# Performance work log

Hardware: AMD Instinct MI355X
Metric: run time of the kernel (lower is better)

Reference implementation:

```python
import jax, jax.numpy as jnp
import numpy as np

B = 32768


def _mk(key, shape, scale=0.05):
    return (jax.random.normal(key, shape, dtype=jnp.float32) * scale)


def setup_inputs() -> dict:
    key = jax.random.key(0)
    ks = jax.random.split(key, 24)
    inp = {
        "p_i": jax.random.normal(ks[0], (B, 512), dtype=jnp.float32),
        "speed": jax.random.normal(ks[1], (B,), dtype=jnp.float32),
        "command": jax.random.randint(ks[2], (B,), 0, 4),
        "sp_W1": _mk(ks[3], (1, 128)), "sp_b1": jnp.zeros((128,), jnp.float32),
        "sp_W2": _mk(ks[4], (128, 128)), "sp_b2": jnp.zeros((128,), jnp.float32),
        "sp_W3": _mk(ks[5], (128, 128)), "sp_b3": jnp.zeros((128,), jnp.float32),
        # speed_pred_module: 512 -> 128 -> 128 -> 1
        "vp_W1": _mk(ks[6], (512, 128)), "vp_b1": jnp.zeros((128,), jnp.float32),
        "vp_W2": _mk(ks[7], (128, 128)), "vp_b2": jnp.zeros((128,), jnp.float32),
        "vp_W3": _mk(ks[8], (128, 1)), "vp_b3": jnp.zeros((1,), jnp.float32),
        # join_module: Linear(640, 512)
        "join_W": _mk(ks[9], (640, 512)), "join_b": jnp.zeros((512,), jnp.float32),
        # 4 control heads: 512 -> 256 -> 256 -> 3 (stacked over expert axis e)
        "ctrl_W1": _mk(ks[10], (4, 512, 256)), "ctrl_b1": jnp.zeros((4, 256), jnp.float32),
        "ctrl_W2": _mk(ks[11], (4, 256, 256)), "ctrl_b2": jnp.zeros((4, 256), jnp.float32),
        "ctrl_W3": _mk(ks[12], (4, 256, 3)), "ctrl_b3": jnp.zeros((4, 3), jnp.float32),
    }
    return inp


def _mlp3(x, W1, b1, W2, b2, W3, b3):
    h = jax.nn.relu(x @ W1 + b1)
    h = jax.nn.relu(h @ W2 + b2)
    return h @ W3 + b3


def reference(p_i, speed, command,
              sp_W1, sp_b1, sp_W2, sp_b2, sp_W3, sp_b3,
              vp_W1, vp_b1, vp_W2, vp_b2, vp_W3, vp_b3,
              join_W, join_b,
              ctrl_W1, ctrl_b1, ctrl_W2, ctrl_b2, ctrl_W3, ctrl_b3):
    v = _mlp3(speed[:, None], sp_W1, sp_b1, sp_W2, sp_b2, sp_W3, sp_b3)
    # join: [B, 640] -> [B, 512]
    joined = jnp.concatenate([p_i, v], axis=1) @ join_W + join_b
    # speed prediction [B,1]
    v_p = _mlp3(p_i, vp_W1, vp_b1, vp_W2, vp_b2, vp_W3, vp_b3)
    # command-indexed routing: compute all 4 tiny heads batched, then select.
    h = jax.nn.relu(jnp.einsum('bd,edh->beh', joined, ctrl_W1) + ctrl_b1)  # [B,4,256]
    h = jax.nn.relu(jnp.einsum('beh,ehk->bek', h, ctrl_W2) + ctrl_b2)      # [B,4,256]
    a = jnp.einsum('beh,ehk->bek', h, ctrl_W3) + ctrl_b3                    # [B,4,3]
    action = jnp.take_along_axis(a, command[:, None, None], axis=1)[:, 0, :]  # [B,3]
    return (v_p, action)
```

## Files before the change

kernel.cpp:

```cpp
#include <hip/hip_runtime.h>
#include <stdint.h>

#define NROWS 32768

typedef float f32x4 __attribute__((ext_vector_type(4)));
typedef __bf16 bfx8 __attribute__((ext_vector_type(8)));
typedef unsigned uint4v __attribute__((ext_vector_type(4)));

static __device__ __forceinline__ unsigned short f2bf(float f) {
    unsigned u = __builtin_bit_cast(unsigned, f);
    u += 0x7fffu + ((u >> 16) & 1u);
    return (unsigned short)(u >> 16);
}

static __device__ __forceinline__ f32x4 mfma16(bfx8 a, bfx8 b, f32x4 c) {
    return __builtin_amdgcn_mfma_f32_16x16x32_bf16(a, b, c, 0, 0, 0);
}

static __device__ __forceinline__ int swz(int row, int col) {
    return col ^ ((row & 7) << 3);
}

static constexpr size_t A_AUG_B  = 0;
static constexpr size_t JOINED_B = 41943040;
static constexpr size_t G1_B     = 75497472;
static constexpr size_t WCT_B    = 83886080;
static constexpr size_t SPW2T_B  = 84705280;
static constexpr size_t SPW3T_B  = 84738048;
static constexpr size_t VPW2T_B  = 84770816;
static constexpr size_t VPW3T_B  = 84803584;
static constexpr size_t C1T_B    = 84807680;
static constexpr size_t C2T_B    = 85856256;
static constexpr size_t C3T_B    = 86380544;
static constexpr size_t CNT_B    = 86413312;
static constexpr size_t SORTED_B = 86413376;
static constexpr size_t WS_NEED  = 86937664;

__global__ __launch_bounds__(256) void k_prep(
    const float* joinW, const float* vpW1, const float* spW2, const float* spW3,
    const float* vpW2, const float* vpW3, const float* c1, const float* c2, const float* c3,
    unsigned short* wct, unsigned short* spw2t, unsigned short* spw3t,
    unsigned short* vpw2t, unsigned short* vpw3t,
    unsigned short* c1t, unsigned short* c2t, unsigned short* c3t, int* cnt)
{
    int bid = blockIdx.x, tid = threadIdx.x;
    if (bid == 0 && tid < 16) cnt[tid] = 0;
    int region, idx0;
    if      (bid < 400)  { region = 0; idx0 = bid * 1024; }
    else if (bid < 416)  { region = 1; idx0 = (bid - 400) * 1024; }
    else if (bid < 432)  { region = 2; idx0 = (bid - 416) * 1024; }
    else if (bid < 448)  { region = 3; idx0 = (bid - 432) * 1024; }
    else if (bid < 450)  { region = 4; idx0 = (bid - 448) * 1024; }
    else if (bid < 962)  { region = 5; idx0 = (bid - 450) * 1024; }
    else if (bid < 1218) { region = 6; idx0 = (bid - 962) * 1024; }
    else                 { region = 7; idx0 = (bid - 1218) * 1024; }
    for (int j = 0; j < 4; ++j) {
        int idx = idx0 + tid + j * 256;
        switch (region) {
        case 0: {
            int n = idx / 640, k = idx % 640;
            float v = (n < 512) ? joinW[(size_t)k * 512 + n]
                                : (k < 512 ? vpW1[(size_t)k * 128 + (n - 512)] : 0.f);
            wct[idx] = f2bf(v);
        } break;
        case 1: { int n = idx >> 7, k = idx & 127; spw2t[idx] = f2bf(spW2[k * 128 + n]); } break;
        case 2: { int n = idx >> 7, k = idx & 127; spw3t[idx] = f2bf(spW3[k * 128 + n]); } break;
        case 3: { int n = idx >> 7, k = idx & 127; vpw2t[idx] = f2bf(vpW2[k * 128 + n]); } break;
        case 4: { int n = idx >> 7, k = idx & 127; vpw3t[idx] = f2bf(n == 0 ? vpW3[k] : 0.f); } break;
        case 5: { int e = idx >> 17, rem = idx & 131071, n = rem >> 9, k = rem & 511;
                  c1t[idx] = f2bf(c1[(size_t)e * 131072 + k * 256 + n]); } break;
        case 6: { int e = idx >> 16, rem = idx & 65535, n = rem >> 8, k = rem & 255;
                  c2t[idx] = f2bf(c2[(size_t)e * 65536 + k * 256 + n]); } break;
        case 7: { int e = idx >> 12, rem = idx & 4095, n = rem >> 8, k = rem & 255;
                  c3t[idx] = f2bf(n < 3 ? c3[(size_t)e * 768 + k * 3 + n] : 0.f); } break;
        }
    }
}

__global__ __launch_bounds__(256) void k_sp_convert(
    const float* p_i, const float* speed, const float* spW1, const float* spb1,
    const float* spb2, const float* spb3,
    const unsigned short* spw2t, const unsigned short* spw3t, unsigned short* Aaug)
{
    __shared__ alignas(16) unsigned short h1[128 * 128];
    __shared__ alignas(16) unsigned short h2[128 * 128];
    int bid = blockIdx.x, tid = threadIdx.x;
    int r0 = bid * 128;
#pragma unroll 4
    for (int j = 0; j < 64; ++j) {
        int c = tid + j * 256;
        int row = c >> 7, col4 = (c & 127) * 4;
        f32x4 v = *(const f32x4*)(p_i + (size_t)(r0 + row) * 512 + col4);
        ushort4 o;
        o.x = f2bf(v.x); o.y = f2bf(v.y); o.z = f2bf(v.z); o.w = f2bf(v.w);
        *(ushort4*)(Aaug + (size_t)(r0 + row) * 640 + col4) = o;
    }
    for (int j = 0; j < 64; ++j) {
        int idx = tid + j * 256;
        int row = idx >> 7, col = idx & 127;
        float h = speed[r0 + row] * spW1[col] + spb1[col];
        h = h > 0.f ? h : 0.f;
        h1[row * 128 + swz(row, col)] = f2bf(h);
    }
    __syncthreads();

    int wave = tid >> 6, lane = tid & 63, lq = lane >> 4, lr = lane & 15;
    int wr = wave >> 1, wc = wave & 1;
    f32x4 acc[4][4] = {};
#pragma unroll
    for (int ks = 0; ks < 4; ++ks) {
        bfx8 a[4], b[4];
#pragma unroll
        for (int mt = 0; mt < 4; ++mt) {
            int row = wr * 64 + mt * 16 + lr;
            a[mt] = *(const bfx8*)&h1[row * 128 + swz(row, ks * 32 + lq * 8)];
        }
#pragma unroll
        for (int nt = 0; nt < 4; ++nt) {
            int n = wc * 64 + nt * 16 + lr;
            b[nt] = *(const bfx8*)(spw2t + n * 128 + ks * 32 + lq * 8);
        }
#pragma unroll
        for (int mt = 0; mt < 4; ++mt)
#pragma unroll
            for (int nt = 0; nt < 4; ++nt)
                acc[mt][nt] = mfma16(a[mt], b[nt], acc[mt][nt]);
    }
#pragma unroll
    for (int mt = 0; mt < 4; ++mt)
#pragma unroll
        for (int nt = 0; nt < 4; ++nt)
#pragma unroll
            for (int j = 0; j < 4; ++j) {
                int row = wr * 64 + mt * 16 + lq * 4 + j;
                int col = wc * 64 + nt * 16 + lr;
                float v = acc[mt][nt][j] + spb2[col];
                v = v > 0.f ? v : 0.f;
                h2[row * 128 + swz(row, col)] = f2bf(v);
            }
    __syncthreads();
    f32x4 acc2[4][4] = {};
#pragma unroll
    for (int ks = 0; ks < 4; ++ks) {
        bfx8 a[4], b[4];
#pragma unroll
        for (int mt = 0; mt < 4; ++mt) {
            int row = wr * 64 + mt * 16 + lr;
            a[mt] = *(const bfx8*)&h2[row * 128 + swz(row, ks * 32 + lq * 8)];
        }
#pragma unroll
        for (int nt = 0; nt < 4; ++nt) {
            int n = wc * 64 + nt * 16 + lr;
            b[nt] = *(const bfx8*)(spw3t + n * 128 + ks * 32 + lq * 8);
        }
#pragma unroll
        for (int mt = 0; mt < 4; ++mt)
#pragma unroll
            for (int nt = 0; nt < 4; ++nt)
                acc2[mt][nt] = mfma16(a[mt], b[nt], acc2[mt][nt]);
    }
#pragma unroll
    for (int mt = 0; mt < 4; ++mt)
#pragma unroll
        for (int nt = 0; nt < 4; ++nt)
#pragma unroll
            for (int j = 0; j < 4; ++j) {
                int row = wr * 64 + mt * 16 + lq * 4 + j;
                int col = wc * 64 + nt * 16 + lr;
                Aaug[(size_t)(r0 + row) * 640 + 512 + col] = f2bf(acc2[mt][nt][j] + spb3[col]);
            }
}

__global__ __launch_bounds__(256) void k_scatter(const int* command, int* cnt, int* sorted)
{
    __shared__ int lcnt[4], lbase[4];
    int tid = threadIdx.x;
    int r = blockIdx.x * 256 + tid;
    if (tid < 4) lcnt[tid] = 0;
    __syncthreads();
    int c = command[r] & 3;
    int lpos = atomicAdd(&lcnt[c], 1);
    __syncthreads();
    if (tid < 4) lbase[tid] = atomicAdd(&cnt[tid], lcnt[tid]);
    __syncthreads();
    sorted[c * NROWS + lbase[c] + lpos] = r;
}

__global__ __launch_bounds__(256) void k_join(
    const unsigned short* Aaug, const unsigned short* wct,
    const float* joinb, const float* vpb1, unsigned short* joined, unsigned short* g1)
{
    __shared__ alignas(16) unsigned short At[128 * 64];
    __shared__ alignas(16) unsigned short Bt[128 * 64];
    int d = blockIdx.x;
    int L = (d & 7) * 160 + (d >> 3);
    int m0 = (L / 5) * 128, n0 = (L % 5) * 128;
    int tid = threadIdx.x, wave = tid >> 6, lane = tid & 63, lq = lane >> 4, lr = lane & 15;
    int wr = wave >> 1, wc = wave & 1;
    f32x4 acc[4][4] = {};
#pragma unroll 1
    for (int kt = 0; kt < 10; ++kt) {
#pragma unroll
        for (int c2 = 0; c2 < 4; ++c2) {
            int chunk = c2 * 256 + tid;
            int row = chunk >> 3, slot = chunk & 7;
            uint4v va = *(const uint4v*)(Aaug + (size_t)(m0 + row) * 640 + kt * 64 + slot * 8);
            uint4v vb = *(const uint4v*)(wct + (size_t)(n0 + row) * 640 + kt * 64 + slot * 8);
            *(uint4v*)&At[chunk * 8] = va;
            *(uint4v*)&Bt[chunk * 8] = vb;
        }
        __syncthreads();
#pragma unroll
        for (int ks = 0; ks < 2; ++ks) {
            bfx8 a[4], b[4];
#pragma unroll
            for (int mt = 0; mt < 4; ++mt)
                a[mt] = *(const bfx8*)&At[(wr * 64 + mt * 16 + lr) * 64 + ks * 32 + lq * 8];
#pragma unroll
            for (int nt = 0; nt < 4; ++nt)
                b[nt] = *(const bfx8*)&Bt[(wc * 64 + nt * 16 + lr) * 64 + ks * 32 + lq * 8];
#pragma unroll
            for (int mt = 0; mt < 4; ++mt)
#pragma unroll
                for (int nt = 0; nt < 4; ++nt)
                    acc[mt][nt] = mfma16(a[mt], b[nt], acc[mt][nt]);
        }
        __syncthreads();
    }
#pragma unroll
    for (int mt = 0; mt < 4; ++mt)
#pragma unroll
        for (int nt = 0; nt < 4; ++nt)
#pragma unroll
            for (int j = 0; j < 4; ++j) {
                int row = m0 + wr * 64 + mt * 16 + lq * 4 + j;
                int col = n0 + wc * 64 + nt * 16 + lr;
                float v = acc[mt][nt][j];
                if (col < 512) {
                    joined[(size_t)row * 512 + col] = f2bf(v + joinb[col]);
                } else {
                    v += vpb1[col - 512];
                    v = v > 0.f ? v : 0.f;
                    g1[(size_t)row * 128 + (col - 512)] = f2bf(v);
                }
            }
}

__global__ __launch_bounds__(256) void k_vp(
    const unsigned short* g1, const unsigned short* vpw2t, const unsigned short* vpw3t,
    const float* vpb2, const float* vpb3, float* out_vp)
{
    __shared__ alignas(16) unsigned short gt[128 * 128];
    __shared__ alignas(16) unsigned short h2[128 * 128];
    int bid = blockIdx.x, tid = threadIdx.x;
    int r0 = bid * 128;
#pragma unroll
    for (int c2 = 0; c2 < 8; ++c2) {
        int chunk = c2 * 256 + tid;
        int row = chunk >> 4, slot = chunk & 15;
        int sslot = slot ^ (row & 7);
        uint4v v = *(const uint4v*)(g1 + (size_t)(r0 + row) * 128 + slot * 8);
        *(uint4v*)&gt[row * 128 + sslot * 8] = v;
    }
    __syncthreads();
    int wave = tid >> 6, lane = tid & 63, lq = lane >> 4, lr = lane & 15;
    int wr = wave >> 1, wc = wave & 1;
    f32x4 acc[4][4] = {};
#pragma unroll
    for (int ks = 0; ks < 4; ++ks) {
        bfx8 a[4], b[4];
#pragma unroll
        for (int mt = 0; mt < 4; ++mt) {
            int row = wr * 64 + mt * 16 + lr;
            a[mt] = *(const bfx8*)&gt[row * 128 + swz(row, ks * 32 + lq * 8)];
        }
#pragma unroll
        for (int nt = 0; nt < 4; ++nt) {
            int n = wc * 64 + nt * 16 + lr;
            b[nt] = *(const bfx8*)(vpw2t + n * 128 + ks * 32 + lq * 8);
        }
#pragma unroll
        for (int mt = 0; mt < 4; ++mt)
#pragma unroll
            for (int nt = 0; nt < 4; ++nt)
                acc[mt][nt] = mfma16(a[mt], b[nt], acc[mt][nt]);
    }
#pragma unroll
    for (int mt = 0; mt < 4; ++mt)
#pragma unroll
        for (int nt = 0; nt < 4; ++nt)
#pragma unroll
            for (int j = 0; j < 4; ++j) {
                int row = wr * 64 + mt * 16 + lq * 4 + j;
                int col = wc * 64 + nt * 16 + lr;
                float v = acc[mt][nt][j] + vpb2[col];
                v = v > 0.f ? v : 0.f;
                h2[row * 128 + swz(row, col)] = f2bf(v);
            }
    __syncthreads();
    f32x4 acc2[2] = {};
#pragma unroll
    for (int ks = 0; ks < 4; ++ks) {
        bfx8 b = *(const bfx8*)(vpw3t + lr * 128 + ks * 32 + lq * 8);
#pragma unroll
        for (int mt = 0; mt < 2; ++mt) {
            int row = wave * 32 + mt * 16 + lr;
            bfx8 a = *(const bfx8*)&h2[row * 128 + swz(row, ks * 32 + lq * 8)];
            acc2[mt] = mfma16(a, b, acc2[mt]);
        }
    }
    if (lr == 0) {
#pragma unroll
        for (int mt = 0; mt < 2; ++mt)
#pragma unroll
            for (int j = 0; j < 4; ++j) {
                int row = wave * 32 + mt * 16 + lq * 4 + j;
                out_vp[r0 + row] = acc2[mt][j] + vpb3[0];
            }
    }
}

__global__ __launch_bounds__(512) void k_ctrl(
    const unsigned short* joined, const unsigned short* c1t, const unsigned short* c2t,
    const unsigned short* c3t, const float* b1, const float* b2, const float* b3,
    const int* cnt, const int* sorted, float* out_act)
{
    __shared__ alignas(16) unsigned short hls[128 * 256];
    __shared__ alignas(16) unsigned short Ast[128 * 64];
    __shared__ alignas(16) unsigned short Bst[256 * 64];
    __shared__ int ridx[128];
    int bid = blockIdx.x;
    int e = bid >> 8, i = bid & 255;
    int n_e = cnt[e];
    if (i * 128 >= n_e) return;
    int tid = threadIdx.x;
    if (tid < 128) {
        int g = i * 128 + tid;
        ridx[tid] = sorted[e * NROWS + (g < n_e ? g : n_e - 1)];
    }
    __syncthreads();
    int wave = tid >> 6, lane = tid & 63, lq = lane >> 4, lr = lane & 15;
    int wm = wave & 1, wn = wave >> 1;
    const unsigned short* W1 = c1t + e * (256 * 512);
    const unsigned short* W2 = c2t + e * (256 * 256);
    const unsigned short* W3 = c3t + e * (16 * 256);

    f32x4 acc[4][4] = {};
#pragma unroll 1
    for (int kt = 0; kt < 8; ++kt) {
#pragma unroll
        for (int it = 0; it < 2; ++it) {
            int idx = it * 512 + tid;
            int row = idx >> 3, slot = idx & 7;
            uint4v v = *(const uint4v*)(joined + (size_t)ridx[row] * 512 + kt * 64 + slot * 8);
            *(uint4v*)&Ast[row * 64 + (slot ^ (row & 7)) * 8] = v;
        }
#pragma unroll
        for (int it = 0; it < 4; ++it) {
            int idx = it * 512 + tid;
            int n = idx >> 3, slot = idx & 7;
            uint4v v = *(const uint4v*)(W1 + (size_t)n * 512 + kt * 64 + slot * 8);
            *(uint4v*)&Bst[n * 64 + (slot ^ (n & 7)) * 8] = v;
        }
        __syncthreads();
#pragma unroll
        for (int ks = 0; ks < 2; ++ks) {
            bfx8 a[4], b[4];
#pragma unroll
            for (int mt = 0; mt < 4; ++mt) {
                int row = wm * 64 + mt * 16 + lr;
                a[mt] = *(const bfx8*)&Ast[row * 64 + ((ks * 32 + lq * 8) ^ ((row & 7) << 3))];
            }
#pragma unroll
            for (int nt = 0; nt < 4; ++nt) {
                int n = wn * 64 + nt * 16 + lr;
                b[nt] = *(const bfx8*)&Bst[n * 64 + ((ks * 32 + lq * 8) ^ ((n & 7) << 3))];
            }
#pragma unroll
            for (int mt = 0; mt < 4; ++mt)
#pragma unroll
                for (int nt = 0; nt < 4; ++nt)
                    acc[mt][nt] = mfma16(a[mt], b[nt], acc[mt][nt]);
        }
        __syncthreads();
    }
#pragma unroll
    for (int mt = 0; mt < 4; ++mt)
#pragma unroll
        for (int nt = 0; nt < 4; ++nt)
#pragma unroll
            for (int j = 0; j < 4; ++j) {
                int row = wm * 64 + mt * 16 + lq * 4 + j;
                int col = wn * 64 + nt * 16 + lr;
                float v = acc[mt][nt][j] + b1[e * 256 + col];
                v = v > 0.f ? v : 0.f;
                hls[row * 256 + swz(row, col)] = f2bf(v);
            }
    __syncthreads();

    f32x4 acc2[4][4] = {};
#pragma unroll 1
    for (int kt = 0; kt < 4; ++kt) {
#pragma unroll
        for (int it = 0; it < 4; ++it) {
            int idx = it * 512 + tid;
            int n = idx >> 3, slot = idx & 7;
            uint4v v = *(const uint4v*)(W2 + (size_t)n * 256 + kt * 64 + slot * 8);
            *(uint4v*)&Bst[n * 64 + (slot ^ (n & 7)) * 8] = v;
        }
        __syncthreads();
#pragma unroll
        for (int ks = 0; ks < 2; ++ks) {
            bfx8 a[4], b[4];
#pragma unroll
            for (int mt = 0; mt < 4; ++mt) {
                int row = wm * 64 + mt * 16 + lr;
                a[mt] = *(const bfx8*)&hls[row * 256 + swz(row, kt * 64 + ks * 32 + lq * 8)];
            }
#pragma unroll
            for (int nt = 0; nt < 4; ++nt) {
                int n = wn * 64 + nt * 16 + lr;
                b[nt] = *(const bfx8*)&Bst[n * 64 + ((ks * 32 + lq * 8) ^ ((n & 7) << 3))];
            }
#pragma unroll
            for (int mt = 0; mt < 4; ++mt)
#pragma unroll
                for (int nt = 0; nt < 4; ++nt)
                    acc2[mt][nt] = mfma16(a[mt], b[nt], acc2[mt][nt]);
        }
        __syncthreads();
    }
#pragma unroll
    for (int mt = 0; mt < 4; ++mt)
#pragma unroll
        for (int nt = 0; nt < 4; ++nt)
#pragma unroll
            for (int j = 0; j < 4; ++j) {
                int row = wm * 64 + mt * 16 + lq * 4 + j;
                int col = wn * 64 + nt * 16 + lr;
                float v = acc2[mt][nt][j] + b2[e * 256 + col];
                v = v > 0.f ? v : 0.f;
                hls[row * 256 + swz(row, col)] = f2bf(v);
            }
    __syncthreads();

    {
        f32x4 acc3 = {};
#pragma unroll
        for (int ks = 0; ks < 8; ++ks) {
            int row = wave * 16 + lr;
            bfx8 a = *(const bfx8*)&hls[row * 256 + swz(row, ks * 32 + lq * 8)];
            bfx8 b = *(const bfx8*)(W3 + lr * 256 + ks * 32 + lq * 8);
            acc3 = mfma16(a, b, acc3);
        }
#pragma unroll
        for (int j = 0; j < 4; ++j) {
            int row = wave * 16 + lq * 4 + j;
            int g = i * 128 + row;
            if (lr < 3 && g < n_e)
                out_act[(size_t)ridx[row] * 3 + lr] = acc3[j] + b3[e * 3 + lr];
        }
    }
}

extern "C" void kernel_launch(void* const* d_in, const int* in_sizes, int n_in,
                              void* d_out, int out_size, void* d_ws, size_t ws_size,
                              hipStream_t stream) {
    (void)in_sizes; (void)n_in; (void)out_size;
    if (ws_size < WS_NEED) return;

    const float* p_i    = (const float*)d_in[0];
    const float* speed  = (const float*)d_in[1];
    const int*   command= (const int*)d_in[2];
    const float* sp_W1  = (const float*)d_in[3];
    const float* sp_b1  = (const float*)d_in[4];
    const float* sp_W2  = (const float*)d_in[5];
    const float* sp_b2  = (const float*)d_in[6];
    const float* sp_W3  = (const float*)d_in[7];
    const float* sp_b3  = (const float*)d_in[8];
    const float* vp_W1  = (const float*)d_in[9];
    const float* vp_b1  = (const float*)d_in[10];
    const float* vp_W2  = (const float*)d_in[11];
    const float* vp_b2  = (const float*)d_in[12];
    const float* vp_W3  = (const float*)d_in[13];
    const float* vp_b3  = (const float*)d_in[14];
    const float* join_W = (const float*)d_in[15];
    const float* join_b = (const float*)d_in[16];
    const float* ctrl_W1= (const float*)d_in[17];
    const float* ctrl_b1= (const float*)d_in[18];
    const float* ctrl_W2= (const float*)d_in[19];
    const float* ctrl_b2= (const float*)d_in[20];
    const float* ctrl_W3= (const float*)d_in[21];
    const float* ctrl_b3= (const float*)d_in[22];

    char* ws = (char*)d_ws;
    unsigned short* Aaug   = (unsigned short*)(ws + A_AUG_B);
    unsigned short* joined = (unsigned short*)(ws + JOINED_B);
    unsigned short* g1     = (unsigned short*)(ws + G1_B);
    unsigned short* wct    = (unsigned short*)(ws + WCT_B);
    unsigned short* spw2t  = (unsigned short*)(ws + SPW2T_B);
    unsigned short* spw3t  = (unsigned short*)(ws + SPW3T_B);
    unsigned short* vpw2t  = (unsigned short*)(ws + VPW2T_B);
    unsigned short* vpw3t  = (unsigned short*)(ws + VPW3T_B);
    unsigned short* c1t    = (unsigned short*)(ws + C1T_B);
    unsigned short* c2t    = (unsigned short*)(ws + C2T_B);
    unsigned short* c3t    = (unsigned short*)(ws + C3T_B);
    int* cnt    = (int*)(ws + CNT_B);
    int* sorted = (int*)(ws + SORTED_B);

    float* out_vp  = (float*)d_out;
    float* out_act = out_vp + NROWS;

    k_prep<<<1234, 256, 0, stream>>>(join_W, vp_W1, sp_W2, sp_W3, vp_W2, vp_W3,
                                     ctrl_W1, ctrl_W2, ctrl_W3,
                                     wct, spw2t, spw3t, vpw2t, vpw3t, c1t, c2t, c3t, cnt);
    k_sp_convert<<<256, 256, 0, stream>>>(p_i, speed, sp_W1, sp_b1, sp_b2, sp_b3,
                                          spw2t, spw3t, Aaug);
    k_scatter<<<128, 256, 0, stream>>>(command, cnt, sorted);
    k_join<<<1280, 256, 0, stream>>>(Aaug, wct, join_b, vp_b1, joined, g1);
    k_vp<<<256, 256, 0, stream>>>(g1, vpw2t, vpw3t, vp_b2, vp_b3, out_vp);
    k_ctrl<<<1024, 512, 0, stream>>>(joined, c1t, c2t, c3t, ctrl_b1, ctrl_b2, ctrl_b3,
                                     cnt, sorted, out_act);
}
```

Before: 317.8 us.

## Prefetch next K-tile into registers and XOR-swizzle LDS tiles in join GEMM

The join GEMM kernel now loads the next K-tile from global memory into registers while the current tile is being consumed by MFMAs, so global-load latency overlaps compute instead of sitting before each barrier. LDS stores and fragment reads use an XOR swizzle on the 16-byte slot index, keyed by row, to avoid bank conflicts on the strided bfx8 reads. This raises register pressure with eight extra uint4 prefetch registers per thread, which could reduce occupancy.

```diff
diff --git a/kernel.cpp b/kernel.cpp
--- a/kernel.cpp
+++ b/kernel.cpp
@@ -197,28 +197,49 @@
     int m0 = (L / 5) * 128, n0 = (L % 5) * 128;
     int tid = threadIdx.x, wave = tid >> 6, lane = tid & 63, lq = lane >> 4, lr = lane & 15;
     int wr = wave >> 1, wc = wave & 1;
+
+    int r0t = tid >> 3, s0t = tid & 7;
+    int ss = s0t ^ (r0t & 7);
+    const unsigned short* aब = Aaug + (size_t)(m0 + r0t) * 640 + s0t * 8;
+    const unsigned short* bब = wct + (size_t)(n0 + r0t) * 640 + s0t * 8;
+    unsigned short* lA = &At[r0t * 64 + ss * 8];
+    unsigned short* lB = &Bt[r0t * 64 + ss * 8];
+
+    uint4v ra[4], rb[4];
+#pragma unroll
+    for (int c2 = 0; c2 < 4; ++c2) {
+        ra[c2] = *(const uint4v*)(aब + c2 * (32 * 640));
+        rb[c2] = *(const uint4v*)(bब + c2 * (32 * 640));
+    }
     f32x4 acc[4][4] = {};
 #pragma unroll 1
     for (int kt = 0; kt < 10; ++kt) {
 #pragma unroll
         for (int c2 = 0; c2 < 4; ++c2) {
-            int chunk = c2 * 256 + tid;
-            int row = chunk >> 3, slot = chunk & 7;
-            uint4v va = *(const uint4v*)(Aaug + (size_t)(m0 + row) * 640 + kt * 64 + slot * 8);
-            uint4v vb = *(const uint4v*)(wct + (size_t)(n0 + row) * 640 + kt * 64 + slot * 8);
-            *(uint4v*)&At[chunk * 8] = va;
-            *(uint4v*)&Bt[chunk * 8] = vb;
+            *(uint4v*)(lA + c2 * (32 * 64)) = ra[c2];
+            *(uint4v*)(lB + c2 * (32 * 64)) = rb[c2];
         }
         __syncthreads();
+        if (kt < 9) {
+#pragma unroll
+            for (int c2 = 0; c2 < 4; ++c2) {
+                ra[c2] = *(const uint4v*)(aब + c2 * (32 * 640) + (kt + 1) * 64);
+                rb[c2] = *(const uint4v*)(bब + c2 * (32 * 640) + (kt + 1) * 64);
+            }
+        }
 #pragma unroll
         for (int ks = 0; ks < 2; ++ks) {
             bfx8 a[4], b[4];
 #pragma unroll
-            for (int mt = 0; mt < 4; ++mt)
-                a[mt] = *(const bfx8*)&At[(wr * 64 + mt * 16 + lr) * 64 + ks * 32 + lq * 8];
-#pragma unroll
-            for (int nt = 0; nt < 4; ++nt)
-                b[nt] = *(const bfx8*)&Bt[(wc * 64 + nt * 16 + lr) * 64 + ks * 32 + lq * 8];
+            for (int mt = 0; mt < 4; ++mt) {
+                int row = wr * 64 + mt * 16 + lr;
+                a[mt] = *(const bfx8*)&At[row * 64 + ((ks * 32 + lq * 8) ^ ((row & 7) << 3))];
+            }
+#pragma unroll
+            for (int nt = 0; nt < 4; ++nt) {
+                int n = wc * 64 + nt * 16 + lr;
+                b[nt] = *(const bfx8*)&Bt[n * 64 + ((ks * 32 + lq * 8) ^ ((n & 7) << 3))];
+            }
 #pragma unroll
             for (int mt = 0; mt < 4; ++mt)
 #pragma unroll
```

Result: faster. 304.5 us (-4.2%).
